# Kernel optimization log

Measured on AMD Instinct MI355X. Metric: run time of the kernel, lower is better.

Reference implementation:

```python
import jax, jax.numpy as jnp
import numpy as np

I, H, T, B, T2 = 512, 1024, 384, 128, 384  # input_size, hidden, cell seq, batch, gru seq


def _gru_layer(x, h0, Wih, Whh, bih, bhh):
    """PyTorch-style GRU layer. x: (B,T,Cin), h0: (B,H). Returns (out (B,T,H), h_last (B,H))."""
    xg = jnp.einsum('btc,gc->btg', x, Wih) + bih  # (B,T,3H) input projections, precomputed

    def step(h, xg_t):
        gh = h @ Whh.T + bhh                      # (B,3H)
        xr, xz, xn = jnp.split(xg_t, 3, axis=-1)
        hr, hz, hn = jnp.split(gh, 3, axis=-1)
        r = jax.nn.sigmoid(xr + hr)
        z = jax.nn.sigmoid(xz + hz)
        n = jnp.tanh(xn + r * hn)
        h_new = (1.0 - z) * n + z * h
        return h_new, h_new

    h_last, ys = jax.lax.scan(step, h0, jnp.swapaxes(xg, 0, 1))  # scan over T
    return jnp.swapaxes(ys, 0, 1), h_last


def setup_inputs() -> dict:
    key = jax.random.key(0)
    ks = jax.random.split(key, 16)
    bound = 1.0 / np.sqrt(H)
    u = lambda kk, shape: jax.random.uniform(kk, shape, jnp.float32, -bound, bound)
    return {
        'input_seq': jax.random.normal(ks[0], (T, B, I), jnp.float32),
        'rand_input': jax.random.normal(ks[1], (B, T2, H), jnp.float32),
        'h0': jax.random.normal(ks[2], (2, B, H), jnp.float32),
        'cell_Wih': u(ks[3], (3 * H, I)),
        'cell_Whh': u(ks[4], (3 * H, H)),
        'cell_bih': u(ks[5], (3 * H,)),
        'cell_bhh': u(ks[6], (3 * H,)),
        'gru_Wih0': u(ks[7], (3 * H, H)),
        'gru_Whh0': u(ks[8], (3 * H, H)),
        'gru_bih0': u(ks[9], (3 * H,)),
        'gru_bhh0': u(ks[10], (3 * H,)),
        'gru_Wih1': u(ks[11], (3 * H, H)),
        'gru_Whh1': u(ks[12], (3 * H, H)),
        'gru_bih1': u(ks[13], (3 * H,)),
        'gru_bhh1': u(ks[14], (3 * H,)),
        'lin_W': u(ks[15], (1, H)),
        'lin_b': jnp.zeros((1,), jnp.float32),
    }


def reference(input_seq, rand_input, h0,
              cell_Wih, cell_Whh, cell_bih, cell_bhh,
              gru_Wih0, gru_Whh0, gru_bih0, gru_bhh0,
              gru_Wih1, gru_Whh1, gru_bih1, gru_bhh1,
              lin_W, lin_b):
    # --- GRUCellModel: cell called with hx=None each step -> hidden is zeros every
    # step, so the whole 'recurrence' vectorizes over T (h @ Whh == 0).
    xg = jnp.einsum('tbi,gi->tbg', input_seq, cell_Wih) + cell_bih  # (T,B,3H)
    xr, xz, xn = jnp.split(xg, 3, axis=-1)
    br, bz, bn = jnp.split(cell_bhh, 3)
    r = jax.nn.sigmoid(xr + br)
    z = jax.nn.sigmoid(xz + bz)
    n = jnp.tanh(xn + r * bn)
    gru_cell_output = jnp.swapaxes((1.0 - z) * n, 0, 1)  # (B,T,H); unused downstream (as in source)

    # --- GRUModel: ignores its input, runs 2-layer GRU on internal random tensors.
    out0, _ = _gru_layer(rand_input, h0[0], gru_Wih0, gru_Whh0, gru_bih0, gru_bhh0)
    gru_output, _ = _gru_layer(out0, h0[1], gru_Wih1, gru_Whh1, gru_bih1, gru_bhh1)

    s = gru_output.shape[1] // 3
    outputs = jnp.concatenate([gru_output[:, 0:s], gru_output[:, s:2 * s], gru_output[:, 2 * s:]], axis=1)

    # second GRU run, zero initial hidden; keep last layer's final hidden
    zero_h = jnp.zeros((outputs.shape[0], H), outputs.dtype)
    o0, _ = _gru_layer(outputs, zero_h, gru_Wih0, gru_Whh0, gru_bih0, gru_bhh0)
    _, h_last = _gru_layer(o0, zero_h, gru_Wih1, gru_Whh1, gru_bih1, gru_bhh1)

    predictions = h_last @ lin_W.T + lin_b  # (B,1)
    # anchor: keep the (dead-code) GRUCell branch alive under jit without changing values
    predictions = predictions + 0.0 * jnp.sum(gru_cell_output)
    return predictions
```

## Files before the change

### kernel.cpp

```cpp
#include <hip/hip_runtime.h>
#include <math.h>

typedef __attribute__((ext_vector_type(8))) __bf16          bf16x8;
typedef __attribute__((ext_vector_type(8))) unsigned short  ushort8;
typedef __attribute__((ext_vector_type(4))) float           f32x4;
typedef __attribute__((ext_vector_type(4))) unsigned int    u32x4;

constexpr int Bb = 128, Hh = 1024, Tt = 384, BH = Bb * Hh;
constexpr int NWG = 256, BLK = 256;

constexpr size_t SLOT_B  = 524288;
constexpr size_t OFF_H   = 1024;
constexpr size_t OFF_W   = OFF_H + 8 * SLOT_B;
constexpr size_t WBLK_B  = 24576;
constexpr size_t OFF_X   = OFF_W + 2048ull * WBLK_B;
constexpr size_t WS_FULL = OFF_X + 384ull * SLOT_B;

__device__ __forceinline__ float b2f(unsigned short h) {
    unsigned u = ((unsigned)h) << 16;
    return __builtin_bit_cast(float, u);
}
__device__ __forceinline__ void split_bf16(float x, unsigned short& hi, unsigned short& lo) {
    unsigned u  = __builtin_bit_cast(unsigned, x);
    unsigned uh = u & 0xFFFF0000u;
    hi = (unsigned short)(uh >> 16);
    float rem = x - __builtin_bit_cast(float, uh);
    unsigned ur = __builtin_bit_cast(unsigned, rem);
    ur += 0x7FFFu + ((ur >> 16) & 1u);
    lo = (unsigned short)(ur >> 16);
}
__device__ __forceinline__ void split8(const float* src, ushort8& h8, ushort8& l8) {
    const float4* p4 = (const float4*)src;
    float4 a = p4[0], b = p4[1];
    float v[8] = {a.x, a.y, a.z, a.w, b.x, b.y, b.z, b.w};
    #pragma unroll
    for (int m = 0; m < 8; ++m) { unsigned short h, l; split_bf16(v[m], h, l); h8[m] = h; l8[m] = l; }
}
__device__ __forceinline__ void async16(const void* g, void* l) {
    __builtin_amdgcn_global_load_lds(
        (const __attribute__((address_space(1))) unsigned int*)g,
        (__attribute__((address_space(3))) unsigned int*)l, 16, 0, 0);
}


__global__ void wsplit_kernel(const float* __restrict__ W0i, const float* __restrict__ W0h,
                              const float* __restrict__ W1i, const float* __restrict__ W1h,
                              char* __restrict__ wbuf) {
    int t = blockIdx.x * 256 + threadIdx.x;
    if (t >= 2048 * 96 * 8) return;
    int g8 = t & 7;
    int r  = (t >> 3) % 96;
    int rest = (t >> 3) / 96;
    int kcg = rest & 15, cg = (rest >> 4) & 31, m = rest >> 9;
    const float* W = (m == 0) ? W0i : (m == 1) ? W0h : (m == 2) ? W1i : W1h;
    int ct = r >> 4, jl = r & 15;
    int jh = ct / 3, g = ct % 3;
    const float* src = W + (size_t)((g << 10) + cg * 32 + jh * 16 + jl) * 1024 + kcg * 64 + g8 * 8;
    ushort8 h8, l8; split8(src, h8, l8);
    int ks = (g8 >> 2) & 1, kg = g8 & 3, lane = kg * 16 + jl;
    char* blk = wbuf + (size_t)rest * WBLK_B;
    int off0 = (ct * 4 + ks) * 1024 + lane * 16;
    *(ushort8*)(blk + off0)        = h8;
    *(ushort8*)(blk + off0 + 2048) = l8;
}

__global__ void xsplit_kernel(const float* __restrict__ xin, char* __restrict__ xb) {
    int t = blockIdx.x * 256 + threadIdx.x;
    if (t >= 384 * 128 * 128) return;
    int g8 = t & 127, b = (t >> 7) & 127, tau = t >> 14;
    const float* src = xin + ((size_t)b * 384 + tau) * 1024 + g8 * 8;
    ushort8 h8, l8; split8(src, h8, l8);
    int kcg = g8 >> 3, gin = g8 & 7;
    int ks = (gin >> 2) & 1, kg = gin & 3;
    int lane = kg * 16 + (b & 15);
    int BI0 = kcg * 32 + (b >> 5) * 8 + ((b >> 4) & 1) * 4 + ks;
    char* dst = xb + (size_t)tau * SLOT_B + (size_t)BI0 * 1024 + lane * 16;
    *(ushort8*)dst          = h8;
    *(ushort8*)(dst + 2048) = l8;
}

__global__ void hinit_kernel(const float* __restrict__ h0, char* __restrict__ ws) {
    int t = blockIdx.x * 256 + threadIdx.x;
    if (t == 0) *(unsigned*)ws = 0;
    if (t >= 4 * 128 * 128) return;
    char* hs = ws + OFF_H;
    int g8 = t & 127, b = (t >> 7) & 127, si = t >> 14;
    ushort8 h8, l8;
    if (si < 2) {
        split8(h0 + (size_t)si * BH + (size_t)b * 1024 + g8 * 8, h8, l8);
    } else {
        #pragma unroll
        for (int m = 0; m < 8; ++m) { h8[m] = 0; l8[m] = 0; }
    }
    int kcg = g8 >> 3, gin = g8 & 7;
    int ks = (gin >> 2) & 1, kg = gin & 3;
    int lane = kg * 16 + (b & 15);
    int BI0 = kcg * 32 + (b >> 5) * 8 + ((b >> 4) & 1) * 4 + ks;
    char* dst = hs + (size_t)(si * 2 + 1) * SLOT_B + (size_t)BI0 * 1024 + lane * 16;
    *(ushort8*)dst          = h8;
    *(ushort8*)(dst + 2048) = l8;
}


__device__ __forceinline__ void grid_barrier(unsigned* cnt, unsigned target) {
    __syncthreads();
    if (threadIdx.x == 0) {
        __hip_atomic_fetch_add(cnt, 1u, __ATOMIC_RELEASE, __HIP_MEMORY_SCOPE_AGENT);
        while (__hip_atomic_load(cnt, __ATOMIC_RELAXED, __HIP_MEMORY_SCOPE_AGENT) < target)
            __builtin_amdgcn_s_sleep(1);
    }
    __syncthreads();
}

#define WAITVM(N) asm volatile("s_waitcnt vmcnt(" #N ")" ::: "memory")

#define GITER(CH, SLOT, ACC, WN, DOISS)                                  \
    WAITVM(WN);                                                          \
    asm volatile("" ::: "memory");                                       \
    __builtin_amdgcn_s_barrier();                                        \
    __builtin_amdgcn_sched_barrier(0);                                   \
    if (DOISS) { issueA((CH) + 3, ar[((SLOT) + 3) & 3]);                 \
                 issueB((CH) + 3, ((SLOT) + 3) & 3); }                   \
    computeC(ar[SLOT], (SLOT), ACC);

template<bool XS>
__global__ __launch_bounds__(BLK, 1) void gru_persistent(
    const float* __restrict__ xin,
    const float* __restrict__ bih0, const float* __restrict__ bhh0,
    const float* __restrict__ bih1, const float* __restrict__ bhh1,
    unsigned* __restrict__ cnt, char* __restrict__ ws)
{
    __shared__ char Bs[4][24576];

    char*       hs = ws + OFF_H;
    const char* wb = ws + OFF_W;
    const char* xs = ws + OFF_X;

    const int bid = blockIdx.x;
    const int xcd = bid & 7, sl = bid >> 3;
    const int pair = xcd * 16 + (sl >> 1), rq = sl & 1;
    const int layer = pair >> 5, cg = pair & 31;
    const int tid = threadIdx.x, lane = tid & 63, wv = tid >> 6;

    const float* bih = (layer & 1) ? bih1 : bih0;
    const float* bhh = (layer & 1) ? bhh1 : bhh0;
    const int jl = lane & 15;

    int   kcg_j[2], ks_j[2], kg_j[2], e_j[2];
    float b_ir[2], b_hr[2], b_iz[2], b_hz[2], b_in[2], b_hn[2];
    #pragma unroll
    for (int jh = 0; jh < 2; ++jh) {
        int j = cg * 32 + jh * 16 + jl;
        kcg_j[jh] = j >> 6; ks_j[jh] = (j >> 5) & 1; kg_j[jh] = (j >> 3) & 3; e_j[jh] = j & 7;
        b_ir[jh] = bih[j];           b_hr[jh] = bhh[j];
        b_iz[jh] = bih[Hh + j];      b_hz[jh] = bhh[Hh + j];
        b_in[jh] = bih[2 * Hh + j];  b_hn[jh] = bhh[2 * Hh + j];
    }
    const int rowBI = (rq * 2 + (wv >> 1)) * 8 + (wv & 1) * 4;

    auto hoff = [&](int jh, int pl, int q) -> size_t {
        return (size_t)(kcg_j[jh] * 32 + rowBI + pl * 2 + ks_j[jh]) * 1024
             + (size_t)(kg_j[jh] * 16 + (lane >> 4) * 4 + q) * 16 + e_j[jh] * 2;
    };

    float hreg[8];
    const bool fb0 = (!XS) && (layer == 0);

    unsigned target = NWG;
    for (int s = 0; s < Tt + 3; ++s, target += NWG) {
        const int tau = s - layer;
        if (tau >= 0 && tau < Tt) {
            const char* Axb = (layer == 0) ? (xs + (size_t)tau * SLOT_B)
                                           : (hs + (size_t)(((layer - 1) * 2) + (tau & 1)) * SLOT_B);
            const char* Ahb = hs + (size_t)((layer * 2) + ((tau - 1) & 1)) * SLOT_B;
            char*       Hd  = hs + (size_t)((layer * 2) + (tau & 1)) * SLOT_B;

            if (tau == 0) {
                if (layer < 2) {
                    #pragma unroll
                    for (int jh = 0; jh < 2; ++jh)
                        #pragma unroll
                        for (int q = 0; q < 4; ++q) {
                            unsigned short hi = __hip_atomic_load(
                                (const unsigned short*)(Ahb + hoff(jh, 0, q)),
                                __ATOMIC_RELAXED, __HIP_MEMORY_SCOPE_AGENT);
                            unsigned short lo = __hip_atomic_load(
                                (const unsigned short*)(Ahb + hoff(jh, 1, q)),
                                __ATOMIC_RELAXED, __HIP_MEMORY_SCOPE_AGENT);
                            hreg[jh * 4 + q] = b2f(hi) + b2f(lo);
                        }
                    asm volatile("s_waitcnt vmcnt(0)" ::: "memory");
                } else {
                    #pragma unroll
                    for (int i = 0; i < 8; ++i) hreg[i] = 0.f;
                }
            }

            auto issueA = [&](int ch, u32x4* fr) {
                const char* p = ((ch < 16) ? Axb : Ahb)
                              + ((size_t)(ch & 15) << 15) + ((size_t)rowBI << 10) + (lane << 4);
                if (!(ch < 16 && layer == 0)) {
                    asm volatile("global_load_dwordx4 %0, %1, off sc0 sc1"             : "=v"(fr[0]) : "v"(p));
                    asm volatile("global_load_dwordx4 %0, %1, off offset:1024 sc0 sc1" : "=v"(fr[1]) : "v"(p));
                    asm volatile("global_load_dwordx4 %0, %1, off offset:2048 sc0 sc1" : "=v"(fr[2]) : "v"(p));
                    asm volatile("global_load_dwordx4 %0, %1, off offset:3072 sc0 sc1" : "=v"(fr[3]) : "v"(p));
                } else {
                    asm volatile("global_load_dwordx4 %0, %1, off"             : "=v"(fr[0]) : "v"(p));
                    asm volatile("global_load_dwordx4 %0, %1, off offset:1024" : "=v"(fr[1]) : "v"(p));
                    asm volatile("global_load_dwordx4 %0, %1, off offset:2048" : "=v"(fr[2]) : "v"(p));
                    asm volatile("global_load_dwordx4 %0, %1, off offset:3072" : "=v"(fr[3]) : "v"(p));
                }
            };
            auto issueB = [&](int ch, int buf) {
                const int m = (layer & 1) * 2 + (ch < 16 ? 0 : 1);
                const char* Wb = wb + (size_t)(((m * 32 + cg) << 4) + (ch & 15)) * WBLK_B;
                char* L = &Bs[buf][0];
                #pragma unroll
                for (int i = 0; i < 6; ++i) {
                    int seg = wv + i * 4;
                    async16(Wb + seg * 1024 + lane * 16, L + seg * 1024);
                }
            };
            auto fragX = [&](int ch, u32x4* fr) {
                const int kcg = ch & 15;
                #pragma unroll
                for (int ks = 0; ks < 2; ++ks) {
                    int row = rq * 64 + wv * 16 + (lane & 15);
                    int k0  = kcg * 64 + ks * 32 + (lane >> 4) * 8;
                    ushort8 h8, l8;
                    split8(xin + ((size_t)row * 384 + tau) * 1024 + k0, h8, l8);
                    fr[ks]     = __builtin_bit_cast(u32x4, h8);
                    fr[2 + ks] = __builtin_bit_cast(u32x4, l8);
                }
            };
            auto computeC = [&](u32x4* fr, int buf, f32x4 (&acc)[6]) {
                const char* B = &Bs[buf][0];
                __builtin_amdgcn_s_setprio(1);
                #pragma unroll
                for (int ks = 0; ks < 2; ++ks) {
                    bf16x8 Ah = __builtin_bit_cast(bf16x8, fr[ks]);
                    bf16x8 Al = __builtin_bit_cast(bf16x8, fr[2 + ks]);
                    #pragma unroll
                    for (int ct = 0; ct < 6; ++ct) {
                        bf16x8 Bh = __builtin_bit_cast(bf16x8, *(const ushort8*)(B + (ct*4 + ks)*1024 + lane*16));
                        bf16x8 Bl = __builtin_bit_cast(bf16x8, *(const ushort8*)(B + (ct*4 + ks)*1024 + 2048 + lane*16));
                        f32x4 c = acc[ct];
                        c = __builtin_amdgcn_mfma_f32_16x16x32_bf16(Ah, Bh, c, 0, 0, 0);
                        c = __builtin_amdgcn_mfma_f32_16x16x32_bf16(Al, Bh, c, 0, 0, 0);
                        c = __builtin_amdgcn_mfma_f32_16x16x32_bf16(Ah, Bl, c, 0, 0, 0);
                        acc[ct] = c;
                    }
                }
                __builtin_amdgcn_s_setprio(0);
            };

            f32x4 accX[6], accH[6];
            const f32x4 zv = {0.f, 0.f, 0.f, 0.f};
            #pragma unroll
            for (int ct = 0; ct < 6; ++ct) { accX[ct] = zv; accH[ct] = zv; }

            u32x4 ar[4][4];

            if (!fb0) {
                issueA(0, ar[0]); issueB(0, 0);
                issueA(1, ar[1]); issueB(1, 1);
                issueA(2, ar[2]); issueB(2, 2);
                for (int c4 = 0; c4 < 16; c4 += 4) {
                    GITER(c4 + 0, 0, accX, 20, true);
                    GITER(c4 + 1, 1, accX, 20, true);
                    GITER(c4 + 2, 2, accX, 20, true);
                    GITER(c4 + 3, 3, accX, 20, true);
                }
                for (int c4 = 16; c4 < 28; c4 += 4) {
                    GITER(c4 + 0, 0, accH, 20, true);
                    GITER(c4 + 1, 1, accH, 20, true);
                    GITER(c4 + 2, 2, accH, 20, true);
                    GITER(c4 + 3, 3, accH, 20, true);
                }
                GITER(28, 0, accH, 20, true);
                GITER(29, 1, accH, 20, false);
                GITER(30, 2, accH, 10, false);
                GITER(31, 3, accH, 0,  false);
            } else {
                for (int ch = 0; ch < 32; ++ch) {
                    if (ch < 16) fragX(ch, ar[0]); else issueA(ch, ar[0]);
                    issueB(ch, 0);
                    asm volatile("s_waitcnt vmcnt(0)" ::: "memory");
                    asm volatile("" ::: "memory");
                    __builtin_amdgcn_s_barrier();
                    __builtin_amdgcn_sched_barrier(0);
                    if (ch < 16) computeC(ar[0], 0, accX); else computeC(ar[0], 0, accH);
                    asm volatile("" ::: "memory");
                    __builtin_amdgcn_s_barrier();
                    asm volatile("" ::: "memory");
                }
            }

            #pragma unroll
            for (int jh = 0; jh < 2; ++jh)
                #pragma unroll
                for (int q = 0; q < 4; ++q) {
                    float rp = accX[jh*3 + 0][q] + accH[jh*3 + 0][q] + b_ir[jh] + b_hr[jh];
                    float zp = accX[jh*3 + 1][q] + accH[jh*3 + 1][q] + b_iz[jh] + b_hz[jh];
                    float xn = accX[jh*3 + 2][q] + b_in[jh];
                    float hn = accH[jh*3 + 2][q] + b_hn[jh];
                    float r  = 1.0f / (1.0f + expf(-rp));
                    float z  = 1.0f / (1.0f + expf(-zp));
                    float n  = tanhf(xn + r * hn);
                    float h  = (1.0f - z) * n + z * hreg[jh * 4 + q];
                    hreg[jh * 4 + q] = h;
                    unsigned short hi, lo; split_bf16(h, hi, lo);
                    __hip_atomic_store((unsigned short*)(Hd + hoff(jh, 0, q)), hi,
                                       __ATOMIC_RELAXED, __HIP_MEMORY_SCOPE_AGENT);
                    __hip_atomic_store((unsigned short*)(Hd + hoff(jh, 1, q)), lo,
                                       __ATOMIC_RELAXED, __HIP_MEMORY_SCOPE_AGENT);
                }
        }
        grid_barrier(cnt, target);
    }
}

__global__ void pred_kernel(const char* __restrict__ hs,
                            const float* __restrict__ linW,
                            const float* __restrict__ linb,
                            float* __restrict__ out) {
    const int b = blockIdx.x, l = threadIdx.x;
    const char* slot = hs + 7 * SLOT_B;
    const int rpart = (b >> 5) * 8 + ((b >> 4) & 1) * 4;
    float s = 0.f;
    for (int u = l; u < Hh; u += 64) {
        int BI0 = (u >> 6) * 32 + rpart + ((u >> 5) & 1);
        size_t o = (size_t)BI0 * 1024 + (size_t)(((u >> 3) & 3) * 16 + (b & 15)) * 16 + (u & 7) * 2;
        float hv = b2f(*(const unsigned short*)(slot + o))
                 + b2f(*(const unsigned short*)(slot + o + 2048));
        s += hv * linW[u];
    }
    #pragma unroll
    for (int off = 32; off > 0; off >>= 1) s += __shfl_down(s, off);
    if (l == 0) out[b] = s + linb[0];
}

extern "C" void kernel_launch(void* const* d_in, const int* in_sizes, int n_in,
                              void* d_out, int out_size, void* d_ws, size_t ws_size,
                              hipStream_t stream) {
    const float* rand_in = (const float*)d_in[1];
    const float* h0      = (const float*)d_in[2];
    const float* Wih0    = (const float*)d_in[7];
    const float* Whh0    = (const float*)d_in[8];
    const float* bih0    = (const float*)d_in[9];
    const float* bhh0    = (const float*)d_in[10];
    const float* Wih1    = (const float*)d_in[11];
    const float* Whh1    = (const float*)d_in[12];
    const float* bih1    = (const float*)d_in[13];
    const float* bhh1    = (const float*)d_in[14];
    const float* linW    = (const float*)d_in[15];
    const float* linb    = (const float*)d_in[16];
    float* out = (float*)d_out;

    char*     ws  = (char*)d_ws;
    unsigned* cnt = (unsigned*)d_ws;
    char*     hsl = ws + OFF_H;

    const bool xsl = (ws_size >= WS_FULL);

    wsplit_kernel<<<6144, 256, 0, stream>>>(Wih0, Whh0, Wih1, Whh1, ws + OFF_W);
    hinit_kernel<<<256, 256, 0, stream>>>(h0, ws);
    if (xsl) {
        xsplit_kernel<<<24576, 256, 0, stream>>>(rand_in, ws + OFF_X);
        gru_persistent<true><<<NWG, BLK, 0, stream>>>(rand_in, bih0, bhh0, bih1, bhh1, cnt, ws);
    } else {
        gru_persistent<false><<<NWG, BLK, 0, stream>>>(rand_in, bih0, bhh0, bih1, bhh1, cnt, ws);
    }
    pred_kernel<<<Bb, 64, 0, stream>>>(hsl, linW, linb, out);
}
```

Measured before the change: 14.96 ms.

## Merge row-quarter workgroup pairs into 512-thread blocks, halving grid size

Work is now split across 128 workgroups of 512 threads instead of 256 workgroups of 256 threads. Each block covers the full 128-row batch for one layer and column group, so the two blocks that previously loaded identical weight tiles now share one LDS copy. Each wave issues half as many weight async loads, and the vmcnt wait thresholds are adjusted to match. The fallback path now double-buffers LDS by chunk parity, which removes the trailing barrier. Fewer workgroups should make the per-step grid barrier cheaper, but only half the CUs are now used and each CU carries eight waves, so register pressure and latency hiding may change.

Measured after the change: 17.37 ms. 1.16x slower.

```diff
diff --git a/kernel.cpp b/kernel.cpp
--- a/kernel.cpp
+++ b/kernel.cpp
@@ -7,7 +7,7 @@
 typedef __attribute__((ext_vector_type(4))) unsigned int    u32x4;
 
 constexpr int Bb = 128, Hh = 1024, Tt = 384, BH = Bb * Hh;
-constexpr int NWG = 256, BLK = 256;
+constexpr int NWG = 128, BLK = 512;
 
 constexpr size_t SLOT_B  = 524288;
 constexpr size_t OFF_H   = 1024;
@@ -119,12 +119,12 @@
     asm volatile("" ::: "memory");                                       \
     __builtin_amdgcn_s_barrier();                                        \
     __builtin_amdgcn_sched_barrier(0);                                   \
-    if (DOISS) { issueA((CH) + 3, ar[((SLOT) + 3) & 3]);                 \
+    if (DOISS) { issueA((CH) + 3, arA[((SLOT) + 3) & 3]);                \
                  issueB((CH) + 3, ((SLOT) + 3) & 3); }                   \
-    computeC(ar[SLOT], (SLOT), ACC);
-
-template<bool XS>
-__global__ __launch_bounds__(BLK, 1) void gru_persistent(
+    computeC(arA[SLOT], (SLOT), ACC);
+
+template<int MODE>
+__global__ __launch_bounds__(BLK, 2) void gru_persistent(
     const float* __restrict__ xin,
     const float* __restrict__ bih0, const float* __restrict__ bhh0,
     const float* __restrict__ bih1, const float* __restrict__ bhh1,
@@ -136,10 +136,7 @@
     const char* wb = ws + OFF_W;
     const char* xs = ws + OFF_X;
 
-    const int bid = blockIdx.x;
-    const int xcd = bid & 7, sl = bid >> 3;
-    const int pair = xcd * 16 + (sl >> 1), rq = sl & 1;
-    const int layer = pair >> 5, cg = pair & 31;
+    const int bid = blockIdx.x, layer = bid >> 5, cg = bid & 31, jbase = cg * 32;
     const int tid = threadIdx.x, lane = tid & 63, wv = tid >> 6;
 
     const float* bih = (layer & 1) ? bih1 : bih0;
@@ -150,13 +147,13 @@
     float b_ir[2], b_hr[2], b_iz[2], b_hz[2], b_in[2], b_hn[2];
     #pragma unroll
     for (int jh = 0; jh < 2; ++jh) {
-        int j = cg * 32 + jh * 16 + jl;
+        int j = jbase + jh * 16 + jl;
         kcg_j[jh] = j >> 6; ks_j[jh] = (j >> 5) & 1; kg_j[jh] = (j >> 3) & 3; e_j[jh] = j & 7;
         b_ir[jh] = bih[j];           b_hr[jh] = bhh[j];
         b_iz[jh] = bih[Hh + j];      b_hz[jh] = bhh[Hh + j];
         b_in[jh] = bih[2 * Hh + j];  b_hn[jh] = bhh[2 * Hh + j];
     }
-    const int rowBI = (rq * 2 + (wv >> 1)) * 8 + (wv & 1) * 4;
+    const int rowBI = (wv >> 1) * 8 + (wv & 1) * 4;
 
     auto hoff = [&](int jh, int pl, int q) -> size_t {
         return (size_t)(kcg_j[jh] * 32 + rowBI + pl * 2 + ks_j[jh]) * 1024
@@ -164,7 +161,7 @@
     };
 
     float hreg[8];
-    const bool fb0 = (!XS) && (layer == 0);
+    const bool fb0 = (MODE == 0) && (layer == 0);
 
     unsigned target = NWG;
     for (int s = 0; s < Tt + 3; ++s, target += NWG) {
@@ -199,7 +196,8 @@
             auto issueA = [&](int ch, u32x4* fr) {
                 const char* p = ((ch < 16) ? Axb : Ahb)
                               + ((size_t)(ch & 15) << 15) + ((size_t)rowBI << 10) + (lane << 4);
-                if (!(ch < 16 && layer == 0)) {
+                const bool coh = !(ch < 16 && layer == 0);
+                if (coh) {
                     asm volatile("global_load_dwordx4 %0, %1, off sc0 sc1"             : "=v"(fr[0]) : "v"(p));
                     asm volatile("global_load_dwordx4 %0, %1, off offset:1024 sc0 sc1" : "=v"(fr[1]) : "v"(p));
                     asm volatile("global_load_dwordx4 %0, %1, off offset:2048 sc0 sc1" : "=v"(fr[2]) : "v"(p));
@@ -216,8 +214,8 @@
                 const char* Wb = wb + (size_t)(((m * 32 + cg) << 4) + (ch & 15)) * WBLK_B;
                 char* L = &Bs[buf][0];
                 #pragma unroll
-                for (int i = 0; i < 6; ++i) {
-                    int seg = wv + i * 4;
+                for (int i = 0; i < 3; ++i) {
+                    int seg = wv + i * 8;
                     async16(Wb + seg * 1024 + lane * 16, L + seg * 1024);
                 }
             };
@@ -225,7 +223,7 @@
                 const int kcg = ch & 15;
                 #pragma unroll
                 for (int ks = 0; ks < 2; ++ks) {
-                    int row = rq * 64 + wv * 16 + (lane & 15);
+                    int row = wv * 16 + (lane & 15);
                     int k0  = kcg * 64 + ks * 32 + (lane >> 4) * 8;
                     ushort8 h8, l8;
                     split8(xin + ((size_t)row * 384 + tau) * 1024 + k0, h8, l8);
@@ -233,13 +231,13 @@
                     fr[2 + ks] = __builtin_bit_cast(u32x4, l8);
                 }
             };
-            auto computeC = [&](u32x4* fr, int buf, f32x4 (&acc)[6]) {
+            auto computeC = [&](u32x4* fa, int buf, f32x4 (&acc)[6]) {
                 const char* B = &Bs[buf][0];
                 __builtin_amdgcn_s_setprio(1);
                 #pragma unroll
                 for (int ks = 0; ks < 2; ++ks) {
-                    bf16x8 Ah = __builtin_bit_cast(bf16x8, fr[ks]);
-                    bf16x8 Al = __builtin_bit_cast(bf16x8, fr[2 + ks]);
+                    bf16x8 Ah = __builtin_bit_cast(bf16x8, fa[ks]);
+                    bf16x8 Al = __builtin_bit_cast(bf16x8, fa[2 + ks]);
                     #pragma unroll
                     for (int ct = 0; ct < 6; ++ct) {
                         bf16x8 Bh = __builtin_bit_cast(bf16x8, *(const ushort8*)(B + (ct*4 + ks)*1024 + lane*16));
@@ -259,40 +257,38 @@
             #pragma unroll
             for (int ct = 0; ct < 6; ++ct) { accX[ct] = zv; accH[ct] = zv; }
 
-            u32x4 ar[4][4];
+            u32x4 arA[4][4];
 
             if (!fb0) {
-                issueA(0, ar[0]); issueB(0, 0);
-                issueA(1, ar[1]); issueB(1, 1);
-                issueA(2, ar[2]); issueB(2, 2);
+                issueA(0, arA[0]); issueB(0, 0);
+                issueA(1, arA[1]); issueB(1, 1);
+                issueA(2, arA[2]); issueB(2, 2);
                 for (int c4 = 0; c4 < 16; c4 += 4) {
-                    GITER(c4 + 0, 0, accX, 20, true);
-                    GITER(c4 + 1, 1, accX, 20, true);
-                    GITER(c4 + 2, 2, accX, 20, true);
-                    GITER(c4 + 3, 3, accX, 20, true);
+                    GITER(c4 + 0, 0, accX, 14, true);
+                    GITER(c4 + 1, 1, accX, 14, true);
+                    GITER(c4 + 2, 2, accX, 14, true);
+                    GITER(c4 + 3, 3, accX, 14, true);
                 }
                 for (int c4 = 16; c4 < 28; c4 += 4) {
-                    GITER(c4 + 0, 0, accH, 20, true);
-                    GITER(c4 + 1, 1, accH, 20, true);
-                    GITER(c4 + 2, 2, accH, 20, true);
-                    GITER(c4 + 3, 3, accH, 20, true);
-                }
-                GITER(28, 0, accH, 20, true);
-                GITER(29, 1, accH, 20, false);
-                GITER(30, 2, accH, 10, false);
+                    GITER(c4 + 0, 0, accH, 14, true);
+                    GITER(c4 + 1, 1, accH, 14, true);
+                    GITER(c4 + 2, 2, accH, 14, true);
+                    GITER(c4 + 3, 3, accH, 14, true);
+                }
+                GITER(28, 0, accH, 14, true);
+                GITER(29, 1, accH, 14, false);
+                GITER(30, 2, accH, 7,  false);
                 GITER(31, 3, accH, 0,  false);
             } else {
                 for (int ch = 0; ch < 32; ++ch) {
-                    if (ch < 16) fragX(ch, ar[0]); else issueA(ch, ar[0]);
-                    issueB(ch, 0);
-                    asm volatile("s_waitcnt vmcnt(0)" ::: "memory");
+                    if (ch < 16) fragX(ch, arA[0]); else issueA(ch, arA[0]);
+                    issueB(ch, ch & 1);
+                    WAITVM(0);
                     asm volatile("" ::: "memory");
                     __builtin_amdgcn_s_barrier();
                     __builtin_amdgcn_sched_barrier(0);
-                    if (ch < 16) computeC(ar[0], 0, accX); else computeC(ar[0], 0, accH);
-                    asm volatile("" ::: "memory");
-                    __builtin_amdgcn_s_barrier();
-                    asm volatile("" ::: "memory");
+                    if (ch < 16) computeC(arA[0], ch & 1, accX);
+                    else         computeC(arA[0], ch & 1, accH);
                 }
             }
 
@@ -320,12 +316,11 @@
     }
 }
 
-__global__ void pred_kernel(const char* __restrict__ hs,
+__global__ void pred_kernel(const char* __restrict__ slot,
                             const float* __restrict__ linW,
                             const float* __restrict__ linb,
                             float* __restrict__ out) {
     const int b = blockIdx.x, l = threadIdx.x;
-    const char* slot = hs + 7 * SLOT_B;
     const int rpart = (b >> 5) * 8 + ((b >> 4) & 1) * 4;
     float s = 0.f;
     for (int u = l; u < Hh; u += 64) {
@@ -367,9 +362,9 @@
     hinit_kernel<<<256, 256, 0, stream>>>(h0, ws);
     if (xsl) {
         xsplit_kernel<<<24576, 256, 0, stream>>>(rand_in, ws + OFF_X);
-        gru_persistent<true><<<NWG, BLK, 0, stream>>>(rand_in, bih0, bhh0, bih1, bhh1, cnt, ws);
+        gru_persistent<1><<<NWG, BLK, 0, stream>>>(rand_in, bih0, bhh0, bih1, bhh1, cnt, ws);
     } else {
-        gru_persistent<false><<<NWG, BLK, 0, stream>>>(rand_in, bih0, bhh0, bih1, bhh1, cnt, ws);
-    }
-    pred_kernel<<<Bb, 64, 0, stream>>>(hsl, linW, linb, out);
-}
+        gru_persistent<0><<<NWG, BLK, 0, stream>>>(rand_in, bih0, bhh0, bih1, bhh1, cnt, ws);
+    }
+    pred_kernel<<<Bb, 64, 0, stream>>>(hsl + 7 * SLOT_B, linW, linb, out);
+}
```
